# Optimization experiments

Measured on AMD Instinct MI355X. Metric: run time of the kernel, lower is better.

The kernel has to match this reference:

```python
import jax, jax.numpy as jnp
import numpy as np


def setup_inputs() -> dict:
    key = jax.random.key(0)
    k1, k2, k3 = jax.random.split(key, 3)
    B, C, H, W = 16, 32, 48, 48
    inp = jax.random.normal(k1, (B, C, H, W), dtype=jnp.float32)
    # weight channels encode a CxC matrix per pixel; add identity (in the
    # flattened C*C channel layout) so every per-pixel matrix is well
    # conditioned for solve/slogdet, as a trained flow's weights would be.
    w = jax.random.normal(k2, (B, C * C, H, W), dtype=jnp.float32) * 0.1
    eye = jnp.eye(C, dtype=jnp.float32).reshape(C * C, 1, 1)
    w = w + eye
    logdet = jax.random.normal(k3, (B,), dtype=jnp.float32)
    return {"input": inp, "weight": w, "logdet": logdet}


def reference(input, weight, logdet):
    # forward (reverse=False) path of InvConditionalLinear
    B, C, H, W = input.shape
    # [B, C*C, H, W] -> [B, H, W, C, C] per-pixel matrices
    w = jnp.transpose(weight, (0, 2, 3, 1)).reshape(B, H, W, C, C)
    # sum of per-pixel log|det W| over all pixels -> [B]
    weight_logdet = jnp.sum(jnp.linalg.slogdet(w)[1], axis=(1, 2))
    # batched per-pixel solve: W z = x
    rhs = jnp.transpose(input, (0, 2, 3, 1))[..., None]  # [B,H,W,C,1]
    z = jnp.linalg.solve(w, rhs)[..., 0]                  # [B,H,W,C]
    z = jnp.transpose(z, (0, 3, 1, 2))                    # [B,C,H,W]
    return z, logdet - weight_logdet
```

## Files before the change

kernel.cpp:

```cpp
#include <hip/hip_runtime.h>
#include <math.h>

#define CDIM 32
#define HWDIM 2304
#define BDIM 16
#define PPW 8
#define NTHREADS 256
#define PPB 32
#define ZOFF (BDIM * CDIM * HWDIM)

__global__ __launch_bounds__(NTHREADS, 2)
void solve_kernel(const float* __restrict__ input,
                  const float* __restrict__ weight,
                  const float* __restrict__ logdet,
                  float* __restrict__ out) {
    const int t    = threadIdx.x;
    const int lane = t & 63;
    const int wv   = t >> 6;
    const int h    = lane & 7;
    const int p    = lane >> 3;
    const int gb   = lane & 56;

    const int blk  = blockIdx.x;
    const int b    = blk / (HWDIM / PPB);
    const int pix0 = (blk % (HWDIM / PPB)) * PPB + wv * PPW;
    const int pix  = pix0 + p;

    const float* wp = weight + (size_t)b * (CDIM * CDIM) * HWDIM
                             + (size_t)(h * CDIM) * HWDIM + pix;
    const float* xp = input + (size_t)b * CDIM * HWDIM + (size_t)h * HWDIM + pix;

    float A[4][CDIM];
    float y[4];
    #pragma unroll
    for (int r = 0; r < 4; ++r) {
        #pragma unroll
        for (int j = 0; j < CDIM; ++j)
            A[r][j] = wp[(size_t)(r * 8 * CDIM + j) * HWDIM];
        y[r] = xp[(size_t)(r * 8) * HWDIM];
    }

    float lacc = 0.0f;
    #pragma unroll
    for (int k = 0; k < CDIM; ++k) {
        const int tr = k >> 3, k7 = k & 7;
        const int src = gb + k7;
        float bp = __shfl(A[tr][k], src);
        float r  = __builtin_amdgcn_rcpf(bp);
        lacc += __log2f(fabsf(bp));

        float m[4];
        m[tr] = (h > k7) ? A[tr][k] * r : ((h == k7) ? (1.0f - r) : 0.0f);
        #pragma unroll
        for (int q = tr + 1; q < 4; ++q) m[q] = A[q][k] * r;

        #pragma unroll
        for (int j = k + 1; j < CDIM; ++j) {
            float bv = __shfl(A[tr][j], src);
            #pragma unroll
            for (int q = tr; q < 4; ++q)
                A[q][j] = fmaf(-m[q], bv, A[q][j]);
        }
        float bq = __shfl(y[tr], src);
        #pragma unroll
        for (int q = tr; q < 4; ++q) y[q] = fmaf(-m[q], bq, y[q]);
    }

    #pragma unroll
    for (int k = CDIM - 1; k >= 1; --k) {
        const int tr = k >> 3, k7 = k & 7;
        const int src = gb + k7;
        float bz = __shfl(y[tr], src);
        float c = (h < k7) ? A[tr][k] : 0.0f;
        y[tr] = fmaf(-c, bz, y[tr]);
        #pragma unroll
        for (int q = 0; q < tr; ++q)
            y[q] = fmaf(-A[q][k], bz, y[q]);
    }

    float* zp = out + (size_t)b * CDIM * HWDIM + (size_t)h * HWDIM + pix;
    #pragma unroll
    for (int r = 0; r < 4; ++r) zp[(size_t)(r * 8) * HWDIM] = y[r];

    float v = lacc;
    v += __shfl_xor(v, 8);
    v += __shfl_xor(v, 16);
    v += __shfl_xor(v, 32);
    if (lane == 0) {
        float add = -v * 0.69314718055994531f;
        if (pix0 == 0) add += logdet[b];
        atomicAdd(&out[ZOFF + b], add);
    }
}

extern "C" void kernel_launch(void* const* d_in, const int* in_sizes, int n_in,
                              void* d_out, int out_size, void* d_ws, size_t ws_size,
                              hipStream_t stream) {
    const float* input  = (const float*)d_in[0];
    const float* weight = (const float*)d_in[1];
    const float* logdet = (const float*)d_in[2];
    float* out = (float*)d_out;

    solve_kernel<<<BDIM * (HWDIM / PPB), NTHREADS, 0, stream>>>(input, weight,
                                                                logdet, out);
}
```

Baseline: 256.5 us.

## Stage weight loads through swizzled LDS with float4 coalesced global reads

```diff
diff --git a/kernel.cpp b/kernel.cpp
--- a/kernel.cpp
+++ b/kernel.cpp
@@ -23,21 +23,59 @@
 
     const int blk  = blockIdx.x;
     const int b    = blk / (HWDIM / PPB);
-    const int pix0 = (blk % (HWDIM / PPB)) * PPB + wv * PPW;
-    const int pix  = pix0 + p;
+    const int pb   = (blk % (HWDIM / PPB)) * PPB;
+    const int pixl = wv * PPW + p;
+    const int pix0 = pb + wv * PPW;
+    const int pix  = pb + pixl;
 
-    const float* wp = weight + (size_t)b * (CDIM * CDIM) * HWDIM
-                             + (size_t)(h * CDIM) * HWDIM + pix;
+    __shared__ float lds[256 * CDIM];
+
     const float* xp = input + (size_t)b * CDIM * HWDIM + (size_t)h * HWDIM + pix;
+    float y[4];
+    #pragma unroll
+    for (int r = 0; r < 4; ++r) y[r] = xp[(size_t)(r * 8) * HWDIM];
+
+    const int sg = lane >> 3;
+    const int sp = lane & 7;
+    const int ps = pixl >> 2, pc = pixl & 3;
+    const float* wbase = weight + (size_t)b * (CDIM * CDIM) * HWDIM + pb;
 
     float A[4][CDIM];
-    float y[4];
+    float4 v[8];
+
+    #pragma unroll
+    for (int q = 0; q < 8; ++q) {
+        const int rcl = wv * 64 + q * 8 + sg;
+        v[q] = *reinterpret_cast<const float4*>(wbase + (size_t)rcl * HWDIM + 4 * sp);
+    }
+
     #pragma unroll
     for (int r = 0; r < 4; ++r) {
+        if (r > 0) {
+            asm volatile("s_waitcnt lgkmcnt(0)" ::: "memory");
+            __builtin_amdgcn_s_barrier();
+            asm volatile("" ::: "memory");
+        }
+        #pragma unroll
+        for (int q = 0; q < 8; ++q) {
+            const int rcl = wv * 64 + q * 8 + sg;
+            *reinterpret_cast<float4*>(
+                &lds[rcl * CDIM + ((sp ^ (rcl >> 5)) << 2)]) = v[q];
+        }
+        if (r < 3) {
+            #pragma unroll
+            for (int q = 0; q < 8; ++q) {
+                const int rcl = wv * 64 + q * 8 + sg;
+                v[q] = *reinterpret_cast<const float4*>(
+                    wbase + (size_t)((r + 1) * 256 + rcl) * HWDIM + 4 * sp);
+            }
+        }
+        asm volatile("s_waitcnt lgkmcnt(0)" ::: "memory");
+        __builtin_amdgcn_s_barrier();
+        asm volatile("" ::: "memory");
         #pragma unroll
         for (int j = 0; j < CDIM; ++j)
-            A[r][j] = wp[(size_t)(r * 8 * CDIM + j) * HWDIM];
-        y[r] = xp[(size_t)(r * 8) * HWDIM];
+            A[r][j] = lds[(h * CDIM + j) * CDIM + ((ps ^ h) << 2) + pc];
     }
 
     float lacc = 0.0f;
@@ -82,12 +120,12 @@
     #pragma unroll
     for (int r = 0; r < 4; ++r) zp[(size_t)(r * 8) * HWDIM] = y[r];
 
-    float v = lacc;
-    v += __shfl_xor(v, 8);
-    v += __shfl_xor(v, 16);
-    v += __shfl_xor(v, 32);
+    float v2 = lacc;
+    v2 += __shfl_xor(v2, 8);
+    v2 += __shfl_xor(v2, 16);
+    v2 += __shfl_xor(v2, 32);
     if (lane == 0) {
-        float add = -v * 0.69314718055994531f;
+        float add = -v2 * 0.69314718055994531f;
         if (pix0 == 0) add += logdet[b];
         atomicAdd(&out[ZOFF + b], add);
     }
```

Result: slower. 273.8 us (+6.8%).
